# Kernel optimization log

Hardware: AMD Instinct MI355X
Metric: run time of the kernel (lower is better)

Reference implementation:

```python
import jax, jax.numpy as jnp
import numpy as np
import math

WINDOW_SIZE = 11
SIGMA = 1.5
CHANNELS = 3
C1 = 0.01 ** 2
C2 = 0.03 ** 2
PAD = WINDOW_SIZE // 2


def make_window():
    # 1D gaussian, normalized, then outer product -> (C, 1, K, K) depthwise kernel
    xs = np.arange(WINDOW_SIZE)
    g = np.exp(-((xs - WINDOW_SIZE // 2) ** 2) / (2.0 * SIGMA ** 2))
    g = (g / g.sum()).astype(np.float32)
    w2d = np.outer(g, g)  # (K, K)
    w = np.broadcast_to(w2d[None, None], (CHANNELS, 1, WINDOW_SIZE, WINDOW_SIZE))
    return jnp.asarray(np.ascontiguousarray(w))


def _dwconv(x, window):
    # depthwise conv2d, groups = channels, 'same' padding for odd K
    return jax.lax.conv_general_dilated(
        x, window,
        window_strides=(1, 1),
        padding=[(PAD, PAD), (PAD, PAD)],
        dimension_numbers=("NCHW", "OIHW", "NCHW"),
        feature_group_count=CHANNELS,
    )


def _ssim_loss(img1, img2, window):
    mu1 = _dwconv(img1, window)
    mu2 = _dwconv(img2, window)
    mu1_sq = mu1 * mu1
    mu2_sq = mu2 * mu2
    mu1_mu2 = mu1 * mu2
    sigma1_sq = _dwconv(img1 * img1, window) - mu1_sq
    sigma2_sq = _dwconv(img2 * img2, window) - mu2_sq
    sigma12 = _dwconv(img1 * img2, window) - mu1_mu2
    ssim_map = ((2.0 * mu1_mu2 + C1) * (2.0 * sigma12 + C2)) / (
        (mu1_sq + mu2_sq + C1) * (sigma1_sq + sigma2_sq + C2)
    )
    return 1.0 - jnp.mean(ssim_map)  # reduction='mean'


def setup_inputs() -> dict:
    key = jax.random.key(0)
    k1, k2 = jax.random.split(key)
    B, C, H, W = 4, 3, 1088, 1920
    img1 = jax.random.uniform(k1, (B, C, H, W), dtype=jnp.float32)
    img2 = jax.random.uniform(k2, (B, C, H, W), dtype=jnp.float32)
    window = make_window()
    return {"img1": img1, "img2": img2, "window": window}


def reference(img1, img2, window):
    return _ssim_loss(img1, img2, window)
```

## Files before the change

### kernel.cpp

```cpp
#include <hip/hip_runtime.h>


typedef _Float16 half8  __attribute__((ext_vector_type(8)));
typedef float    f32x4  __attribute__((ext_vector_type(4)));
typedef unsigned int uint4v __attribute__((ext_vector_type(4)));

namespace {
constexpr int IW  = 1920;
constexpr int IH  = 1088;
constexpr int NPL = 12;
constexpr int TW  = 32;
constexpr int TH  = 64;
constexpr int TX  = IW / TW;
constexpr int TY  = IH / TH;
constexpr int NTILE = TX * TY * NPL;
constexpr int NSLOT = 128;
constexpr int SPAD  = 8;
constexpr float C1v = 0.0001f;
constexpr float C2v = 0.0009f;
constexpr double NPIX = 25067520.0;
}

__global__ __launch_bounds__(256)
__attribute__((amdgpu_waves_per_eu(3, 4)))
void ssim_main(const float* __restrict__ img1,
               const float* __restrict__ img2,
               double* __restrict__ acc) {
    const int lane = threadIdx.x & 63;
    const int wv   = threadIdx.x >> 6;
    const int wid  = blockIdx.x * 4 + wv;

    const int tx = wid % TX;
    const int t2 = wid / TX;
    const int ty = t2 % TY;
    const int pl = t2 / TY;

    const int l15 = lane & 15;
    const int lg  = lane >> 4;

    const int X0 = tx * TW;
    const int Y0 = ty * TH - 5;

    const float* __restrict__ base1 = img1 + (long long)pl * IH * IW;
    const float* __restrict__ base2 = img2 + (long long)pl * IH * IW;

    half8 wH, wV;
#pragma unroll
    for (int i = 0; i < 8; ++i) {
        const int k   = lg * 8 + i;
        const int iv  = k - l15;
        const int ih2 = iv - 3;
        const int dv = iv - 5, dh = ih2 - 5;
        const float ev = __expf((float)(dv * dv) * (-1.0f / 4.5f)) * 0.26601172f;
        const float eh = __expf((float)(dh * dh) * (-1.0f / 4.5f)) * 0.26601172f;
        wV[i] = (_Float16)((iv  >= 0 && iv  <= 10) ? ev : 0.0f);
        wH[i] = (_Float16)((ih2 >= 0 && ih2 <= 10) ? eh : 0.0f);
    }

    __shared__ _Float16 ringall[4][5][32][32];
    _Float16* __restrict__ rg = &ringall[wv][0][0][0];

    float sum = 0.0f;
    const f32x4 zz = {0.0f, 0.0f, 0.0f, 0.0f};

    f32x4 pA[4], pB[4];

    auto issue_loads = [&](int g) {
        const int gy = Y0 + 16 * g + l15;
        const bool rowok = ((unsigned)gy < (unsigned)IH);
        const long long rbase = (long long)gy * IW;
        const bool safe = (tx > 0) && (tx < TX - 1) &&
                          !(ty == 0 && g == 0) && !(ty == TY - 1 && g == 4);
        if (safe) {
#pragma unroll
            for (int ct = 0; ct < 2; ++ct) {
                const int gx0 = X0 - 8 + 16 * ct + lg * 8;
                const f32x4* pa = (const f32x4*)(base1 + rbase + gx0);
                const f32x4* pb = (const f32x4*)(base2 + rbase + gx0);
                pA[2 * ct] = pa[0]; pA[2 * ct + 1] = pa[1];
                pB[2 * ct] = pb[0]; pB[2 * ct + 1] = pb[1];
            }
        } else {
#pragma unroll
            for (int ct = 0; ct < 2; ++ct) {
                const int gx0 = X0 - 8 + 16 * ct + lg * 8;
#pragma unroll
                for (int j = 0; j < 2; ++j) {
                    f32x4 va = zz, vb = zz;
                    if (rowok) {
#pragma unroll
                        for (int e = 0; e < 4; ++e) {
                            const int gx = gx0 + 4 * j + e;
                            if (gx >= 0 && gx < IW) {
                                va[e] = base1[rbase + gx];
                                vb[e] = base2[rbase + gx];
                            }
                        }
                    }
                    pA[2 * ct + j] = va;
                    pB[2 * ct + j] = vb;
                }
            }
        }
    };

    auto pack8 = [](f32x4 u, f32x4 v) -> half8 {
        uint4v t;
        t[0] = __builtin_bit_cast(unsigned int, __builtin_amdgcn_cvt_pkrtz(u[0], u[1]));
        t[1] = __builtin_bit_cast(unsigned int, __builtin_amdgcn_cvt_pkrtz(u[2], u[3]));
        t[2] = __builtin_bit_cast(unsigned int, __builtin_amdgcn_cvt_pkrtz(v[0], v[1]));
        t[3] = __builtin_bit_cast(unsigned int, __builtin_amdgcn_cvt_pkrtz(v[2], v[3]));
        return __builtin_bit_cast(half8, t);
    };

    auto store4 = [](_Float16* p, f32x4 c) {
        uint2 u;
        u.x = __builtin_bit_cast(unsigned int, __builtin_amdgcn_cvt_pkrtz(c[0], c[1]));
        u.y = __builtin_bit_cast(unsigned int, __builtin_amdgcn_cvt_pkrtz(c[2], c[3]));
        *(uint2*)p = u;
    };

    auto vtile = [&](int t) {
#pragma unroll
        for (int vc = 0; vc < 2; ++vc) {
            const int col = 16 * vc + l15;
            const int rs0 = (16 * t + lg * 8) & 31;
            const int rbs = (rs0 >> 3) ^ (col & 3);
            const _Float16* rp = rg + col * 32 + rbs * 8;

            const f32x4 a0 = __builtin_amdgcn_mfma_f32_16x16x32_f16(wV, *(const half8*)(rp + 0 * 1024), zz, 0, 0, 0);
            const f32x4 a1 = __builtin_amdgcn_mfma_f32_16x16x32_f16(wV, *(const half8*)(rp + 1 * 1024), zz, 0, 0, 0);
            const f32x4 a2 = __builtin_amdgcn_mfma_f32_16x16x32_f16(wV, *(const half8*)(rp + 2 * 1024), zz, 0, 0, 0);
            const f32x4 a3 = __builtin_amdgcn_mfma_f32_16x16x32_f16(wV, *(const half8*)(rp + 3 * 1024), zz, 0, 0, 0);
            const f32x4 a4 = __builtin_amdgcn_mfma_f32_16x16x32_f16(wV, *(const half8*)(rp + 4 * 1024), zz, 0, 0, 0);

#pragma unroll
            for (int i = 0; i < 4; ++i) {
                const float mu1 = a0[i], mu2 = a1[i];
                const float ea = a2[i], eb = a3[i], eab = a4[i];
                const float mu1s = mu1 * mu1, mu2s = mu2 * mu2, mu12 = mu1 * mu2;
                const float s1 = ea - mu1s, s2 = eb - mu2s, s12 = eab - mu12;
                const float num = (2.0f * mu12 + C1v) * (2.0f * s12 + C2v);
                const float den = (mu1s + mu2s + C1v) * (s1 + s2 + C2v);
                sum += num * __builtin_amdgcn_rcpf(den);
            }
        }
    };

    issue_loads(0);
#pragma clang loop unroll(disable)
    for (int g = 0; g < 5; ++g) {
        half8 af0 = pack8(pA[0], pA[1]), bf0 = pack8(pB[0], pB[1]);
        half8 af1 = pack8(pA[2], pA[3]), bf1 = pack8(pB[2], pB[3]);

        if (g < 4) issue_loads(g + 1);

#pragma unroll
        for (int ct = 0; ct < 2; ++ct) {
            const half8 af = ct ? af1 : af0;
            const half8 bf = ct ? bf1 : bf0;
            const half8 aa = af * af;
            const half8 bb = bf * bf;
            const half8 ab = af * bf;

            const f32x4 c0 = __builtin_amdgcn_mfma_f32_16x16x32_f16(af, wH, zz, 0, 0, 0);
            const f32x4 c1 = __builtin_amdgcn_mfma_f32_16x16x32_f16(bf, wH, zz, 0, 0, 0);
            const f32x4 c2 = __builtin_amdgcn_mfma_f32_16x16x32_f16(aa, wH, zz, 0, 0, 0);
            const f32x4 c3 = __builtin_amdgcn_mfma_f32_16x16x32_f16(bb, wH, zz, 0, 0, 0);
            const f32x4 c4 = __builtin_amdgcn_mfma_f32_16x16x32_f16(ab, wH, zz, 0, 0, 0);

            const int col = 16 * ct + l15;
            const int rs  = (16 * g + lg * 4) & 31;
            const int rbs = (rs >> 3) ^ (col & 3);
            _Float16* wp = rg + col * 32 + rbs * 8 + (rs & 7);
            store4(wp + 0 * 1024, c0);
            store4(wp + 1 * 1024, c1);
            store4(wp + 2 * 1024, c2);
            store4(wp + 3 * 1024, c3);
            store4(wp + 4 * 1024, c4);
        }

        if (g > 0) vtile(g - 1);
    }

#pragma unroll
    for (int off = 32; off > 0; off >>= 1) sum += __shfl_down(sum, off);
    if (lane == 0) atomicAdd(acc + (wid & (NSLOT - 1)) * SPAD, (double)sum);
}

__global__ void ssim_fin(const double* __restrict__ acc, float* __restrict__ out) {
    const int lane = threadIdx.x & 63;
    double s = acc[lane * SPAD] + acc[(lane + 64) * SPAD];
#pragma unroll
    for (int off = 32; off > 0; off >>= 1)
        s += __shfl_down(s, off);
    if (lane == 0) out[0] = 1.0f - (float)(s / NPIX);
}

extern "C" void kernel_launch(void* const* d_in, const int* in_sizes, int n_in,
                              void* d_out, int out_size, void* d_ws, size_t ws_size,
                              hipStream_t stream) {
    (void)in_sizes; (void)n_in; (void)out_size; (void)ws_size;
    const float* img1 = (const float*)d_in[0];
    const float* img2 = (const float*)d_in[1];
    float* out = (float*)d_out;
    double* acc = (double*)d_ws;

    (void)hipMemsetAsync(acc, 0, NSLOT * SPAD * sizeof(double), stream);
    ssim_main<<<dim3(NTILE / 4), dim3(256), 0, stream>>>(img1, img2, acc);
    ssim_fin<<<1, 64, 0, stream>>>(acc, out);
}
```

Baseline: 263.8 us.

## Remove LDS ring by permuting input rows so horizontal MFMA output feeds vertical MFMA

Narrows tiles to 16 columns and reorders the rows each lane loads so that the packed fp16 output of the horizontal-pass MFMA is already in the operand layout the vertical-pass MFMA needs. This removes the shared-memory ring buffer with its stores and reads. Each wave now covers 16x64 outputs in 4 steps, so vertical halo reloads rise as a share of the work. Per-wave atomics are also replaced by a block-level shared reduction with a single atomic per block, and the occupancy hint is raised to 4-8 waves per EU.

```diff
diff --git a/kernel.cpp b/kernel.cpp
--- a/kernel.cpp
+++ b/kernel.cpp
@@ -9,7 +9,7 @@
 constexpr int IW  = 1920;
 constexpr int IH  = 1088;
 constexpr int NPL = 12;
-constexpr int TW  = 32;
+constexpr int TW  = 16;
 constexpr int TH  = 64;
 constexpr int TX  = IW / TW;
 constexpr int TY  = IH / TH;
@@ -22,7 +22,7 @@
 }
 
 __global__ __launch_bounds__(256)
-__attribute__((amdgpu_waves_per_eu(3, 4)))
+__attribute__((amdgpu_waves_per_eu(4, 8)))
 void ssim_main(const float* __restrict__ img1,
                const float* __restrict__ img2,
                double* __restrict__ acc) {
@@ -38,8 +38,8 @@
     const int l15 = lane & 15;
     const int lg  = lane >> 4;
 
-    const int X0 = tx * TW;
-    const int Y0 = ty * TH - 5;
+    const int X0  = tx * TW;
+    const int gx0 = X0 - 8 + lg * 8;
 
     const float* __restrict__ base1 = img1 + (long long)pl * IH * IW;
     const float* __restrict__ base2 = img2 + (long long)pl * IH * IW;
@@ -57,48 +57,41 @@
         wH[i] = (_Float16)((ih2 >= 0 && ih2 <= 10) ? eh : 0.0f);
     }
 
-    __shared__ _Float16 ringall[4][5][32][32];
-    _Float16* __restrict__ rg = &ringall[wv][0][0][0];
-
     float sum = 0.0f;
     const f32x4 zz = {0.0f, 0.0f, 0.0f, 0.0f};
 
-    f32x4 pA[4], pB[4];
+    f32x4 p1[2][2], p2[2][2];
 
     auto issue_loads = [&](int g) {
-        const int gy = Y0 + 16 * g + l15;
-        const bool rowok = ((unsigned)gy < (unsigned)IH);
-        const long long rbase = (long long)gy * IW;
+        const int Yb = ty * TH + g * 16 - 5;
         const bool safe = (tx > 0) && (tx < TX - 1) &&
-                          !(ty == 0 && g == 0) && !(ty == TY - 1 && g == 4);
-        if (safe) {
+                          !(ty == 0 && g == 0) && !(ty == TY - 1 && g == 3);
 #pragma unroll
-            for (int ct = 0; ct < 2; ++ct) {
-                const int gx0 = X0 - 8 + 16 * ct + lg * 8;
-                const f32x4* pa = (const f32x4*)(base1 + rbase + gx0);
-                const f32x4* pb = (const f32x4*)(base2 + rbase + gx0);
-                pA[2 * ct] = pa[0]; pA[2 * ct + 1] = pa[1];
-                pB[2 * ct] = pb[0]; pB[2 * ct + 1] = pb[1];
-            }
-        } else {
-#pragma unroll
-            for (int ct = 0; ct < 2; ++ct) {
-                const int gx0 = X0 - 8 + 16 * ct + lg * 8;
+        for (int c = 0; c < 2; ++c) {
+            const int rr = Yb + ((l15 >> 2) * 8 + c * 4 + (l15 & 3));
+            const long long rb = (long long)rr * IW;
+            if (safe) {
+                const f32x4* pa = (const f32x4*)(base1 + rb + gx0);
+                const f32x4* pb = (const f32x4*)(base2 + rb + gx0);
+                p1[c][0] = pa[0]; p1[c][1] = pa[1];
+                p2[c][0] = pb[0]; p2[c][1] = pb[1];
+            } else {
+                const bool rok = (unsigned)rr < (unsigned)IH;
 #pragma unroll
                 for (int j = 0; j < 2; ++j) {
                     f32x4 va = zz, vb = zz;
-                    if (rowok) {
+                    if (rok) {
 #pragma unroll
                         for (int e = 0; e < 4; ++e) {
                             const int gx = gx0 + 4 * j + e;
                             if (gx >= 0 && gx < IW) {
-                                va[e] = base1[rbase + gx];
-                                vb[e] = base2[rbase + gx];
+                                va[e] = base1[rb + gx];
+                                vb[e] = base2[rb + gx];
                             }
                         }
                     }
-                    pA[2 * ct + j] = va;
-                    pB[2 * ct + j] = vb;
+                    p1[c][j] = va;
+                    p2[c][j] = vb;
                 }
             }
         }
@@ -113,79 +106,61 @@
         return __builtin_bit_cast(half8, t);
     };
 
-    auto store4 = [](_Float16* p, f32x4 c) {
-        uint2 u;
-        u.x = __builtin_bit_cast(unsigned int, __builtin_amdgcn_cvt_pkrtz(c[0], c[1]));
-        u.y = __builtin_bit_cast(unsigned int, __builtin_amdgcn_cvt_pkrtz(c[2], c[3]));
-        *(uint2*)p = u;
-    };
+    issue_loads(0);
+#pragma clang loop unroll(disable)
+    for (int g = 0; g < 4; ++g) {
+        const half8 af0 = pack8(p1[0][0], p1[0][1]);
+        const half8 bf0 = pack8(p2[0][0], p2[0][1]);
+        const half8 af1 = pack8(p1[1][0], p1[1][1]);
+        const half8 bf1 = pack8(p2[1][0], p2[1][1]);
 
-    auto vtile = [&](int t) {
-#pragma unroll
-        for (int vc = 0; vc < 2; ++vc) {
-            const int col = 16 * vc + l15;
-            const int rs0 = (16 * t + lg * 8) & 31;
-            const int rbs = (rs0 >> 3) ^ (col & 3);
-            const _Float16* rp = rg + col * 32 + rbs * 8;
+        if (g < 3) issue_loads(g + 1);
 
-            const f32x4 a0 = __builtin_amdgcn_mfma_f32_16x16x32_f16(wV, *(const half8*)(rp + 0 * 1024), zz, 0, 0, 0);
-            const f32x4 a1 = __builtin_amdgcn_mfma_f32_16x16x32_f16(wV, *(const half8*)(rp + 1 * 1024), zz, 0, 0, 0);
-            const f32x4 a2 = __builtin_amdgcn_mfma_f32_16x16x32_f16(wV, *(const half8*)(rp + 2 * 1024), zz, 0, 0, 0);
-            const f32x4 a3 = __builtin_amdgcn_mfma_f32_16x16x32_f16(wV, *(const half8*)(rp + 3 * 1024), zz, 0, 0, 0);
-            const f32x4 a4 = __builtin_amdgcn_mfma_f32_16x16x32_f16(wV, *(const half8*)(rp + 4 * 1024), zz, 0, 0, 0);
+        f32x4 cA, cB;
+        cA = __builtin_amdgcn_mfma_f32_16x16x32_f16(af0, wH, zz, 0, 0, 0);
+        cB = __builtin_amdgcn_mfma_f32_16x16x32_f16(af1, wH, zz, 0, 0, 0);
+        const half8 h0 = pack8(cA, cB);
+        cA = __builtin_amdgcn_mfma_f32_16x16x32_f16(bf0, wH, zz, 0, 0, 0);
+        cB = __builtin_amdgcn_mfma_f32_16x16x32_f16(bf1, wH, zz, 0, 0, 0);
+        const half8 h1 = pack8(cA, cB);
+        cA = __builtin_amdgcn_mfma_f32_16x16x32_f16(af0 * af0, wH, zz, 0, 0, 0);
+        cB = __builtin_amdgcn_mfma_f32_16x16x32_f16(af1 * af1, wH, zz, 0, 0, 0);
+        const half8 h2 = pack8(cA, cB);
+        cA = __builtin_amdgcn_mfma_f32_16x16x32_f16(bf0 * bf0, wH, zz, 0, 0, 0);
+        cB = __builtin_amdgcn_mfma_f32_16x16x32_f16(bf1 * bf1, wH, zz, 0, 0, 0);
+        const half8 h3 = pack8(cA, cB);
+        cA = __builtin_amdgcn_mfma_f32_16x16x32_f16(af0 * bf0, wH, zz, 0, 0, 0);
+        cB = __builtin_amdgcn_mfma_f32_16x16x32_f16(af1 * bf1, wH, zz, 0, 0, 0);
+        const half8 h4 = pack8(cA, cB);
+
+        const f32x4 a0 = __builtin_amdgcn_mfma_f32_16x16x32_f16(wV, h0, zz, 0, 0, 0);
+        const f32x4 a1 = __builtin_amdgcn_mfma_f32_16x16x32_f16(wV, h1, zz, 0, 0, 0);
+        const f32x4 a2 = __builtin_amdgcn_mfma_f32_16x16x32_f16(wV, h2, zz, 0, 0, 0);
+        const f32x4 a3 = __builtin_amdgcn_mfma_f32_16x16x32_f16(wV, h3, zz, 0, 0, 0);
+        const f32x4 a4 = __builtin_amdgcn_mfma_f32_16x16x32_f16(wV, h4, zz, 0, 0, 0);
 
 #pragma unroll
-            for (int i = 0; i < 4; ++i) {
-                const float mu1 = a0[i], mu2 = a1[i];
-                const float ea = a2[i], eb = a3[i], eab = a4[i];
-                const float mu1s = mu1 * mu1, mu2s = mu2 * mu2, mu12 = mu1 * mu2;
-                const float s1 = ea - mu1s, s2 = eb - mu2s, s12 = eab - mu12;
-                const float num = (2.0f * mu12 + C1v) * (2.0f * s12 + C2v);
-                const float den = (mu1s + mu2s + C1v) * (s1 + s2 + C2v);
-                sum += num * __builtin_amdgcn_rcpf(den);
-            }
+        for (int i = 0; i < 4; ++i) {
+            const float mu1 = a0[i], mu2 = a1[i];
+            const float ea = a2[i], eb = a3[i], eab = a4[i];
+            const float mu1s = mu1 * mu1, mu2s = mu2 * mu2, mu12 = mu1 * mu2;
+            const float s1 = ea - mu1s, s2 = eb - mu2s, s12 = eab - mu12;
+            const float num = (2.0f * mu12 + C1v) * (2.0f * s12 + C2v);
+            const float den = (mu1s + mu2s + C1v) * (s1 + s2 + C2v);
+            sum += num * __builtin_amdgcn_rcpf(den);
         }
-    };
-
-    issue_loads(0);
-#pragma clang loop unroll(disable)
-    for (int g = 0; g < 5; ++g) {
-        half8 af0 = pack8(pA[0], pA[1]), bf0 = pack8(pB[0], pB[1]);
-        half8 af1 = pack8(pA[2], pA[3]), bf1 = pack8(pB[2], pB[3]);
-
-        if (g < 4) issue_loads(g + 1);
-
-#pragma unroll
-        for (int ct = 0; ct < 2; ++ct) {
-            const half8 af = ct ? af1 : af0;
-            const half8 bf = ct ? bf1 : bf0;
-            const half8 aa = af * af;
-            const half8 bb = bf * bf;
-            const half8 ab = af * bf;
-
-            const f32x4 c0 = __builtin_amdgcn_mfma_f32_16x16x32_f16(af, wH, zz, 0, 0, 0);
-            const f32x4 c1 = __builtin_amdgcn_mfma_f32_16x16x32_f16(bf, wH, zz, 0, 0, 0);
-            const f32x4 c2 = __builtin_amdgcn_mfma_f32_16x16x32_f16(aa, wH, zz, 0, 0, 0);
-            const f32x4 c3 = __builtin_amdgcn_mfma_f32_16x16x32_f16(bb, wH, zz, 0, 0, 0);
-            const f32x4 c4 = __builtin_amdgcn_mfma_f32_16x16x32_f16(ab, wH, zz, 0, 0, 0);
-
-            const int col = 16 * ct + l15;
-            const int rs  = (16 * g + lg * 4) & 31;
-            const int rbs = (rs >> 3) ^ (col & 3);
-            _Float16* wp = rg + col * 32 + rbs * 8 + (rs & 7);
-            store4(wp + 0 * 1024, c0);
-            store4(wp + 1 * 1024, c1);
-            store4(wp + 2 * 1024, c2);
-            store4(wp + 3 * 1024, c3);
-            store4(wp + 4 * 1024, c4);
-        }
-
-        if (g > 0) vtile(g - 1);
     }
 
 #pragma unroll
     for (int off = 32; off > 0; off >>= 1) sum += __shfl_down(sum, off);
-    if (lane == 0) atomicAdd(acc + (wid & (NSLOT - 1)) * SPAD, (double)sum);
+
+    __shared__ double bsum[4];
+    if (lane == 0) bsum[wv] = (double)sum;
+    __syncthreads();
+    if (threadIdx.x == 0) {
+        const double s = bsum[0] + bsum[1] + bsum[2] + bsum[3];
+        atomicAdd(acc + (blockIdx.x & (NSLOT - 1)) * SPAD, s);
+    }
 }
 
 __global__ void ssim_fin(const double* __restrict__ acc, float* __restrict__ out) {
```

Measured after the change: 301.8 us. 14.4% more time.
